# Performance work log

Hardware: AMD Instinct MI355X
Metric: run time of the kernel (lower is better)

Reference implementation:

```python
import jax, jax.numpy as jnp
import numpy as np

GROUPS = 8
EPS = 1e-5


def setup_inputs() -> dict:
    key = jax.random.key(0)
    ks = jax.random.split(key, 7)
    b, c, h, w = 32, 256, 32, 32
    x = jax.random.normal(ks[0], (b, c, h, w), dtype=jnp.float32)
    gn_weight = jax.random.normal(ks[1], (c,), dtype=jnp.float32) * 0.02 + 1.0
    gn_bias = jax.random.normal(ks[2], (c,), dtype=jnp.float32) * 0.02
    w_qkv = jax.random.normal(ks[3], (3 * c, c), dtype=jnp.float32) / np.sqrt(c)
    b_qkv = jax.random.normal(ks[4], (3 * c,), dtype=jnp.float32) * 0.01
    w_out = jax.random.normal(ks[5], (c, c), dtype=jnp.float32) / np.sqrt(c)
    b_out = jax.random.normal(ks[6], (c,), dtype=jnp.float32) * 0.01
    return {"x": x, "gn_weight": gn_weight, "gn_bias": gn_bias,
            "w_qkv": w_qkv, "b_qkv": b_qkv, "w_out": w_out, "b_out": b_out}


def group_norm(x, weight, bias):
    b, c, h, w = x.shape
    xg = x.reshape(b, GROUPS, c // GROUPS, h, w)
    mean = jnp.mean(xg, axis=(2, 3, 4), keepdims=True)
    var = jnp.var(xg, axis=(2, 3, 4), keepdims=True)
    xg = (xg - mean) * jax.lax.rsqrt(var + EPS)
    x = xg.reshape(b, c, h, w)
    return x * weight[None, :, None, None] + bias[None, :, None, None]


def reference(x, gn_weight, gn_bias, w_qkv, b_qkv, w_out, b_out):
    b, c, h, w = x.shape
    x_norm = group_norm(x, gn_weight, gn_bias)
    # 1x1 conv == channel matmul: (b, 3c, h, w)
    qkv = jnp.einsum('oc,bchw->bohw', w_qkv, x_norm) + b_qkv[None, :, None, None]
    q, k, v = jnp.split(qkv, 3, axis=1)
    hw = h * w
    q = q.reshape(b, c, hw)  # used transposed: (b, hw, c)
    k = k.reshape(b, c, hw)
    v = v.reshape(b, c, hw)
    scale = 1.0 / jnp.sqrt(jnp.float32(c))
    attn = jax.nn.softmax(jnp.einsum('bcs,bct->bst', q, k) * scale, axis=-1)  # (b, hw, hw)
    out = jnp.einsum('bst,bct->bcs', attn, v).reshape(b, c, h, w)
    out = jnp.einsum('oc,bchw->bohw', w_out, out) + b_out[None, :, None, None]
    return out + x
```

## Files before the change

### kernel.cpp

```cpp
#include <hip/hip_runtime.h>
#include <hip/hip_bf16.h>


typedef __bf16 bf16x8 __attribute__((ext_vector_type(8)));
typedef __bf16 bf16x4 __attribute__((ext_vector_type(4)));
typedef __bf16 bf16x2 __attribute__((ext_vector_type(2)));
typedef float f32x4 __attribute__((ext_vector_type(4)));
typedef float f32x16 __attribute__((ext_vector_type(16)));

#define MFMA16(a, b, c) __builtin_amdgcn_mfma_f32_16x16x32_bf16(a, b, c, 0, 0, 0)
#define MFMA32(a, b, c) __builtin_amdgcn_mfma_f32_32x32x16_bf16(a, b, c, 0, 0, 0)

#define GLD16(gsrc_, ldst_)                                                                  \
    __builtin_amdgcn_global_load_lds((const __attribute__((address_space(1))) void*)(gsrc_), \
                                     (__attribute__((address_space(3))) void*)(ldst_), 16, 0, 0)

__global__ __launch_bounds__(512) void gn_kernel(const float* __restrict__ x,
                                                 const float* __restrict__ gw,
                                                 const float* __restrict__ gb,
                                                 __bf16* __restrict__ xnT,
                                                 const float* __restrict__ wqkv,
                                                 const float* __restrict__ wout,
                                                 __bf16* __restrict__ wbf) {
    __shared__ float red[16];
    __shared__ float stats[2];
    __shared__ __bf16 Lds[512][40];
    const int b = blockIdx.x >> 3, g = blockIdx.x & 7;
    const size_t base = ((size_t)b * 256 + g * 32) * 1024;
    const float* xp = x + base;
    const int t = threadIdx.x;

    {
        int widx = (blockIdx.x * 512 + t) * 2;
        const float* wsrc = (widx < 196608) ? (wqkv + widx) : (wout + (widx - 196608));
        float2 wv = *(const float2*)wsrc;
        bf16x2 wo;
        wo[0] = (__bf16)wv.x; wo[1] = (__bf16)wv.y;
        *(bf16x2*)&wbf[widx] = wo;
    }

    float s = 0.f, s2 = 0.f;
    #pragma unroll
    for (int i = 0; i < 8; i++) {
        int j = i * 512 + t;
        float4 v0 = *(const float4*)(xp + (size_t)j * 8);
        float4 v1 = *(const float4*)(xp + (size_t)j * 8 + 4);
        s  += v0.x + v0.y + v0.z + v0.w + v1.x + v1.y + v1.z + v1.w;
        s2 += v0.x*v0.x + v0.y*v0.y + v0.z*v0.z + v0.w*v0.w
            + v1.x*v1.x + v1.y*v1.y + v1.z*v1.z + v1.w*v1.w;
    }
    #pragma unroll
    for (int o = 32; o > 0; o >>= 1) { s += __shfl_down(s, o, 64); s2 += __shfl_down(s2, o, 64); }
    const int wv = t >> 6;
    if ((t & 63) == 0) { red[wv * 2] = s; red[wv * 2 + 1] = s2; }
    __syncthreads();
    if (t == 0) {
        float ts = 0.f, ts2 = 0.f;
        for (int w = 0; w < 8; w++) { ts += red[w * 2]; ts2 += red[w * 2 + 1]; }
        float mean = ts / 32768.f;
        float var = ts2 / 32768.f - mean * mean;
        stats[0] = mean; stats[1] = rsqrtf(var + 1e-5f);
    }
    __syncthreads();
    const float mean = stats[0], inv = stats[1];

    const int c = t >> 4;
    const int so = (t & 15) * 2;
    const float ga = gw[g * 32 + c], be = gb[g * 32 + c];

    for (int chunk = 0; chunk < 1024; chunk += 512) {
        #pragma unroll
        for (int i = 0; i < 16; i++) {
            int sl = so + i * 32;
            float2 v = *(const float2*)(xp + (size_t)c * 1024 + chunk + sl);
            Lds[sl][c]     = (__bf16)((v.x - mean) * inv * ga + be);
            Lds[sl + 1][c] = (__bf16)((v.y - mean) * inv * ga + be);
        }
        __syncthreads();
        {
            int sl = t;
            #pragma unroll
            for (int u = 0; u < 4; u++) {
                bf16x8 vv = *(const bf16x8*)&Lds[sl][u * 8];
                *(bf16x8*)&xnT[((size_t)b * 1024 + chunk + sl) * 256 + g * 32 + u * 8] = vv;
            }
        }
        __syncthreads();
    }
}

#define GEMM64G_BODY(ArowBase_, BrowBase_)                                              \
    f32x4 acc[4][4] = {};                                                               \
    for (int kk = 0; kk < 256; kk += 64) {                                              \
        _Pragma("unroll")                                                               \
        for (int i = 0; i < 4; i++) {                                                   \
            const int ch = wave * 4 + i;                                                \
            const int r = ch * 8 + (lane >> 3);                                         \
            const int sw = ((lane & 7) ^ (r & 7)) * 8;                                  \
            GLD16((ArowBase_) + (size_t)r * 256 + kk + sw, (char*)&As[0][0] + ch * 1024); \
            GLD16((BrowBase_) + (size_t)r * 256 + kk + sw, (char*)&Bs[0][0] + ch * 1024); \
        }                                                                               \
        __syncthreads();                                                                \
        _Pragma("unroll")                                                               \
        for (int kh = 0; kh < 2; kh++) {                                                \
            bf16x8 af[4], bfv[4];                                                       \
            _Pragma("unroll")                                                           \
            for (int im = 0; im < 4; im++) {                                            \
                const int row = wm + im * 16 + l16;                                     \
                af[im] = *(const bf16x8*)&As[row][(((kh * 4 + quad) ^ (row & 7)) * 8)]; \
            }                                                                           \
            _Pragma("unroll")                                                           \
            for (int in = 0; in < 4; in++) {                                            \
                const int row = wn + in * 16 + l16;                                     \
                bfv[in] = *(const bf16x8*)&Bs[row][(((kh * 4 + quad) ^ (row & 7)) * 8)]; \
            }                                                                           \
            _Pragma("unroll")                                                           \
            for (int im = 0; im < 4; im++)                                              \
                _Pragma("unroll")                                                       \
                for (int in = 0; in < 4; in++)                                          \
                    acc[im][in] = MFMA16(af[im], bfv[in], acc[im][in]);                 \
        }                                                                               \
        __syncthreads();                                                                \
    }

__global__ __launch_bounds__(256) void qkv_gemm(const __bf16* __restrict__ wbf,
                                                const float* __restrict__ bias,
                                                const __bf16* __restrict__ xnT,
                                                __bf16* __restrict__ qtr,
                                                __bf16* __restrict__ ktr,
                                                __bf16* __restrict__ vbuf) {
    __shared__ union {
        struct { __bf16 A[128][64]; __bf16 B[128][64]; } g;
        __bf16 ct[128][136];
    } sm;
    const int b = blockIdx.z;
    const int n0 = blockIdx.x * 128, m0 = blockIdx.y * 128;
    const int t = threadIdx.x;
    const int wave = t >> 6, lane = t & 63, quad = lane >> 4, l16 = lane & 15;
    const int wm = (wave & 1) * 64, wn = (wave >> 1) * 64;
    const __bf16* arow = wbf + (size_t)m0 * 256;
    const __bf16* brow = xnT + ((size_t)b * 1024 + n0) * 256;
    auto As = sm.g.A;
    auto Bs = sm.g.B;

    GEMM64G_BODY(arow, brow)

    if (m0 < 512) {
        #pragma unroll
        for (int im = 0; im < 4; im++) {
            #pragma unroll
            for (int in = 0; in < 4; in++) {
                int ob = m0 + wm + im * 16 + quad * 4;
                bf16x4 ov;
                #pragma unroll
                for (int r = 0; r < 4; r++) ov[r] = (__bf16)(acc[im][in][r] + bias[ob + r]);
                *(bf16x4*)&sm.ct[wn + in * 16 + l16][wm + im * 16 + quad * 4] = ov;
            }
        }
        __syncthreads();
        {
            const int rbase = t >> 2, cf = t & 3;
            #pragma unroll
            for (int rr = 0; rr < 2; rr++) {
                int row = rbase + rr * 64;
                int sg = n0 + row;
                __bf16* dst = (m0 < 256) ? &qtr[((size_t)b * 1024 + sg) * 256 + m0]
                                         : &ktr[((size_t)b * 1024 + sg) * 256 + (m0 - 256)];
                #pragma unroll
                for (int u = 0; u < 4; u++) {
                    int colb = cf * 8 + u * 32;
                    *(bf16x8*)&dst[colb] = *(const bf16x8*)&sm.ct[row][colb];
                }
            }
        }
    } else {
        #pragma unroll
        for (int im = 0; im < 4; im++) {
            #pragma unroll
            for (int in = 0; in < 4; in++) {
                int cl = wm + im * 16 + quad * 4;
                int tl = wn + in * 16 + l16;
                #pragma unroll
                for (int r = 0; r < 4; r++)
                    sm.ct[cl + r][tl] = (__bf16)(acc[im][in][r] + bias[m0 + cl + r]);
            }
        }
        __syncthreads();
        {
            const int row = t >> 1, tc = (t & 1) * 64;
            const int cglob = m0 - 512 + row;
            __bf16* dst = &vbuf[((size_t)b * 256 + cglob) * 1024 + n0 + tc];
            #pragma unroll
            for (int u = 0; u < 8; u++)
                *(bf16x8*)&dst[u * 8] = *(const bf16x8*)&sm.ct[row][tc + u * 8];
        }
    }
}

__global__ __launch_bounds__(512, 2) void attn_kernel(const __bf16* __restrict__ qtr,
                                                      const __bf16* __restrict__ ktr,
                                                      const __bf16* __restrict__ vbuf,
                                                      __bf16* __restrict__ aoT) {
    __shared__ __bf16 Kt[2][32][260];
    __shared__ __bf16 Vs[2][256][36];
    __shared__ bf16x8 Pl[4][2][2][64];
    __shared__ float Lred[4][2][32];
    const int b = blockIdx.x;
    const int tid = threadIdx.x;
    const int wave = tid >> 6, lane = tid & 63, half = lane >> 5, l31 = lane & 31;
    const int pair = wave & 3, th = wave >> 2;
    const int s0 = blockIdx.y * 128 + pair * 32;
    const float kscale = 0.09016844f;

    bf16x8 aq[16];
    #pragma unroll
    for (int ks = 0; ks < 16; ks++)
        aq[ks] = *(const bf16x8*)&qtr[((size_t)b * 1024 + s0 + l31) * 256 + ks * 16 + half * 8];

    const int k_row = tid >> 3;
    const int k_cb  = (tid & 7) * 8;
    const int v_c   = tid >> 1;
    const int v_th  = tid & 1;
    const size_t kbase = (size_t)b * 1024 * 256;
    const size_t vbase = (size_t)b * 256 * 1024;

    float l_acc = 0.f;
    f32x16 o_acc[4] = {};

    bf16x8 kpre[4], vpre[4];
    #pragma unroll
    for (int u = 0; u < 4; u++) {
        kpre[u] = *(const bf16x8*)&ktr[kbase + (size_t)k_row * 256 + k_cb + u * 64];
        vpre[u] = *(const bf16x8*)&vbuf[vbase + (size_t)v_c * 1024 + v_th * 32 + u * 8];
    }

    for (int it = 0; it < 16; it++) {
        #pragma unroll
        for (int u = 0; u < 4; u++)
            *(bf16x8*)&Kt[k_row >> 5][k_row & 31][k_cb + u * 64] = kpre[u];
        #pragma unroll
        for (int u = 0; u < 4; u++) {
            const bf16x4* hv = (const bf16x4*)&vpre[u];
            const int sbase = (u >> 1) * 16 + (u & 1) * 4;
            *(bf16x4*)&Vs[v_th][v_c][sbase]     = hv[0];
            *(bf16x4*)&Vs[v_th][v_c][sbase + 8] = hv[1];
        }
        __syncthreads();
        if (it < 15) {
            const int t1 = (it + 1) * 64;
            #pragma unroll
            for (int u = 0; u < 4; u++) {
                kpre[u] = *(const bf16x8*)&ktr[kbase + (size_t)(t1 + k_row) * 256 + k_cb + u * 64];
                vpre[u] = *(const bf16x8*)&vbuf[vbase + (size_t)v_c * 1024 + t1 + v_th * 32 + u * 8];
            }
        }

        f32x16 sc_a = {}, sc_b = {};
        __builtin_amdgcn_s_setprio(1);
        #pragma unroll
        for (int ks = 0; ks < 8; ks++) {
            bf16x8 bk0 = *(const bf16x8*)&Kt[th][l31][ks * 16 + half * 8];
            bf16x8 bk1 = *(const bf16x8*)&Kt[th][l31][(ks + 8) * 16 + half * 8];
            sc_a = MFMA32(bk0, aq[ks], sc_a);
            sc_b = MFMA32(bk1, aq[ks + 8], sc_b);
        }
        __builtin_amdgcn_s_setprio(0);

        bf16x8 pf0, pf1;
        #pragma unroll
        for (int r = 0; r < 8; r++) {
            float p = exp2f((sc_a[r] + sc_b[r]) * kscale);
            l_acc += p;
            pf0[r] = (__bf16)p;
        }
        #pragma unroll
        for (int r = 8; r < 16; r++) {
            float p = exp2f((sc_a[r] + sc_b[r]) * kscale);
            l_acc += p;
            pf1[r - 8] = (__bf16)p;
        }
        Pl[pair][th][0][lane] = pf0;
        Pl[pair][th][1][lane] = pf1;
        __syncthreads();
        bf16x8 pp0 = Pl[pair][1 - th][0][lane];
        bf16x8 pp1 = Pl[pair][1 - th][1][lane];

        bf16x8 ap[4];
        if (th == 0) { ap[0] = pf0; ap[1] = pf1; ap[2] = pp0; ap[3] = pp1; }
        else         { ap[0] = pp0; ap[1] = pp1; ap[2] = pf0; ap[3] = pf1; }

        __builtin_amdgcn_s_setprio(1);
        #pragma unroll
        for (int n = 0; n < 4; n++) {
            int c = th * 128 + n * 32 + l31;
            #pragma unroll
            for (int kc = 0; kc < 4; kc++) {
                bf16x8 bv = *(const bf16x8*)&Vs[kc >> 1][c][(kc & 1) * 16 + half * 8];
                o_acc[n] = MFMA32(ap[kc], bv, o_acc[n]);
            }
        }
        __builtin_amdgcn_s_setprio(0);
        __syncthreads();
    }

    l_acc += __shfl_xor(l_acc, 32, 64);
    if (lane < 32) Lred[pair][th][l31] = l_acc;
    __syncthreads();
    #pragma unroll
    for (int r = 0; r < 16; r++) {
        int row = (r & 3) + 8 * (r >> 2) + 4 * half;
        float rinv = 1.0f / (Lred[pair][0][row] + Lred[pair][1][row]);
        #pragma unroll
        for (int n = 0; n < 4; n++) {
            int c = th * 128 + n * 32 + l31;
            aoT[((size_t)b * 1024 + s0 + row) * 256 + c] = (__bf16)(o_acc[n][r] * rinv);
        }
    }
}

__global__ __launch_bounds__(256) void proj_gemm(const __bf16* __restrict__ wbf_out,
                                                 const float* __restrict__ bias,
                                                 const __bf16* __restrict__ aoT,
                                                 const float* __restrict__ resid,
                                                 float* __restrict__ Out) {
    __shared__ union {
        struct { __bf16 A[128][64]; __bf16 B[128][64]; } g;
        float cf[64][132];
    } sm;
    const int b = blockIdx.z;
    const int n0 = blockIdx.x * 128, m0 = blockIdx.y * 128;
    const int t = threadIdx.x;
    const int wave = t >> 6, lane = t & 63, quad = lane >> 4, l16 = lane & 15;
    const int wm = (wave & 1) * 64, wn = (wave >> 1) * 64;
    const __bf16* arow = wbf_out + (size_t)m0 * 256;
    const __bf16* brow = aoT + ((size_t)b * 1024 + n0) * 256;
    auto As = sm.g.A;
    auto Bs = sm.g.B;

    GEMM64G_BODY(arow, brow)

    for (int h = 0; h < 2; h++) {
        if ((wave & 1) == h) {
            #pragma unroll
            for (int im = 0; im < 4; im++)
                #pragma unroll
                for (int in = 0; in < 4; in++)
                    #pragma unroll
                    for (int r = 0; r < 4; r++)
                        sm.cf[im * 16 + quad * 4 + r][wn + in * 16 + l16] = acc[im][in][r];
        }
        __syncthreads();
        {
            const int rloc = t >> 2, cq = (t & 3) * 4;
            const int o = m0 + h * 64 + rloc;
            const float bo = bias[o];
            const float* rrow = &resid[((size_t)b * 256 + o) * 1024 + n0];
            float* orow = &Out[((size_t)b * 256 + o) * 1024 + n0];
            #pragma unroll
            for (int u = 0; u < 8; u++) {
                int col = cq + u * 16;
                f32x4 cv = *(const f32x4*)&sm.cf[rloc][col];
                float4 rv = *(const float4*)&rrow[col];
                float4 ov;
                ov.x = cv[0] + bo + rv.x;
                ov.y = cv[1] + bo + rv.y;
                ov.z = cv[2] + bo + rv.z;
                ov.w = cv[3] + bo + rv.w;
                *(float4*)&orow[col] = ov;
            }
        }
        __syncthreads();
    }
}

extern "C" void kernel_launch(void* const* d_in, const int* in_sizes, int n_in,
                              void* d_out, int out_size, void* d_ws, size_t ws_size,
                              hipStream_t stream) {
    const float* x    = (const float*)d_in[0];
    const float* gw   = (const float*)d_in[1];
    const float* gb   = (const float*)d_in[2];
    const float* wqkv = (const float*)d_in[3];
    const float* bqkv = (const float*)d_in[4];
    const float* wout = (const float*)d_in[5];
    const float* bout = (const float*)d_in[6];
    float* out = (float*)d_out;

    const size_t T16 = (size_t)32 * 1024 * 256;
    __bf16* xnT  = (__bf16*)d_ws;
    __bf16* qtr  = xnT + T16;
    __bf16* ktr  = qtr + T16;
    __bf16* vbuf = ktr + T16;
    __bf16* aoT  = vbuf + T16;
    __bf16* wbf  = aoT + T16;

    gn_kernel<<<dim3(256), 512, 0, stream>>>(x, gw, gb, xnT, wqkv, wout, wbf);
    qkv_gemm<<<dim3(8, 6, 32), 256, 0, stream>>>(wbf, bqkv, xnT, qtr, ktr, vbuf);
    attn_kernel<<<dim3(32, 8), 512, 0, stream>>>(qtr, ktr, vbuf, aoT);
    proj_gemm<<<dim3(8, 2, 32), 256, 0, stream>>>(wbf + 196608, bout, aoT, x, out);
}
```

Before: 190.7 us.

## Split group norm into stats and apply kernels; remap GEMM blocks per XCD

The single 256-block group-norm kernel becomes two kernels: a 2048-block partial-stats pass (which also converts the weights to bf16) and a 2048-block apply/transpose pass that reduces the partial sums itself. This raises parallelism across the GPU's CUs, at the cost of one extra launch and reading x twice. The QKV and projection GEMMs also remap their block IDs so that consecutive tiles sharing operand panels land on the same XCD, which should improve L2 reuse.

New measurement: 186.4 us. -2.3%, faster.

```diff
diff --git a/kernel.cpp b/kernel.cpp
--- a/kernel.cpp
+++ b/kernel.cpp
@@ -4,7 +4,6 @@
 
 typedef __bf16 bf16x8 __attribute__((ext_vector_type(8)));
 typedef __bf16 bf16x4 __attribute__((ext_vector_type(4)));
-typedef __bf16 bf16x2 __attribute__((ext_vector_type(2)));
 typedef float f32x4 __attribute__((ext_vector_type(4)));
 typedef float f32x16 __attribute__((ext_vector_type(16)));
 
@@ -15,78 +14,72 @@
     __builtin_amdgcn_global_load_lds((const __attribute__((address_space(1))) void*)(gsrc_), \
                                      (__attribute__((address_space(3))) void*)(ldst_), 16, 0, 0)
 
-__global__ __launch_bounds__(512) void gn_kernel(const float* __restrict__ x,
-                                                 const float* __restrict__ gw,
-                                                 const float* __restrict__ gb,
-                                                 __bf16* __restrict__ xnT,
-                                                 const float* __restrict__ wqkv,
-                                                 const float* __restrict__ wout,
-                                                 __bf16* __restrict__ wbf) {
-    __shared__ float red[16];
-    __shared__ float stats[2];
-    __shared__ __bf16 Lds[512][40];
-    const int b = blockIdx.x >> 3, g = blockIdx.x & 7;
-    const size_t base = ((size_t)b * 256 + g * 32) * 1024;
-    const float* xp = x + base;
-    const int t = threadIdx.x;
-
-    {
-        int widx = (blockIdx.x * 512 + t) * 2;
-        const float* wsrc = (widx < 196608) ? (wqkv + widx) : (wout + (widx - 196608));
-        float2 wv = *(const float2*)wsrc;
-        bf16x2 wo;
-        wo[0] = (__bf16)wv.x; wo[1] = (__bf16)wv.y;
-        *(bf16x2*)&wbf[widx] = wo;
-    }
-
+__global__ __launch_bounds__(256) void gn_stats(const float* __restrict__ x,
+                                                float* __restrict__ stats,
+                                                const float* __restrict__ wqkv,
+                                                const float* __restrict__ wout,
+                                                __bf16* __restrict__ wbf) {
+    const int bid = blockIdx.x, t = threadIdx.x;
+    if (bid < 128) {
+        int idx = (bid * 256 + t) * 8;
+        const float* src = (idx < 196608) ? (wqkv + idx) : (wout + (idx - 196608));
+        float4 v0 = *(const float4*)src;
+        float4 v1 = *(const float4*)(src + 4);
+        bf16x8 o;
+        o[0] = (__bf16)v0.x; o[1] = (__bf16)v0.y; o[2] = (__bf16)v0.z; o[3] = (__bf16)v0.w;
+        o[4] = (__bf16)v1.x; o[5] = (__bf16)v1.y; o[6] = (__bf16)v1.z; o[7] = (__bf16)v1.w;
+        *(bf16x8*)&wbf[idx] = o;
+    }
+    const int bg = bid >> 3, part = bid & 7;
+    const float* xp = x + (size_t)bg * 32768 + part * 4096;
     float s = 0.f, s2 = 0.f;
     #pragma unroll
-    for (int i = 0; i < 8; i++) {
-        int j = i * 512 + t;
-        float4 v0 = *(const float4*)(xp + (size_t)j * 8);
-        float4 v1 = *(const float4*)(xp + (size_t)j * 8 + 4);
-        s  += v0.x + v0.y + v0.z + v0.w + v1.x + v1.y + v1.z + v1.w;
-        s2 += v0.x*v0.x + v0.y*v0.y + v0.z*v0.z + v0.w*v0.w
-            + v1.x*v1.x + v1.y*v1.y + v1.z*v1.z + v1.w*v1.w;
+    for (int i = 0; i < 4; i++) {
+        float4 v = *(const float4*)(xp + (i * 256 + t) * 4);
+        s  += v.x + v.y + v.z + v.w;
+        s2 += v.x*v.x + v.y*v.y + v.z*v.z + v.w*v.w;
     }
     #pragma unroll
     for (int o = 32; o > 0; o >>= 1) { s += __shfl_down(s, o, 64); s2 += __shfl_down(s2, o, 64); }
+    __shared__ float red[8];
     const int wv = t >> 6;
     if ((t & 63) == 0) { red[wv * 2] = s; red[wv * 2 + 1] = s2; }
     __syncthreads();
     if (t == 0) {
-        float ts = 0.f, ts2 = 0.f;
-        for (int w = 0; w < 8; w++) { ts += red[w * 2]; ts2 += red[w * 2 + 1]; }
-        float mean = ts / 32768.f;
-        float var = ts2 / 32768.f - mean * mean;
-        stats[0] = mean; stats[1] = rsqrtf(var + 1e-5f);
-    }
+        float ts  = red[0] + red[2] + red[4] + red[6];
+        float ts2 = red[1] + red[3] + red[5] + red[7];
+        stats[bg * 16 + part * 2]     = ts;
+        stats[bg * 16 + part * 2 + 1] = ts2;
+    }
+}
+
+__global__ __launch_bounds__(512) void gn_apply(const float* __restrict__ x,
+                                                const float* __restrict__ stats,
+                                                const float* __restrict__ gw,
+                                                const float* __restrict__ gb,
+                                                __bf16* __restrict__ xnT) {
+    const int bid = blockIdx.x;
+    const int bg = bid >> 3, part = bid & 7;
+    const int b = bg >> 3, g = bg & 7;
+    const int t = threadIdx.x;
+    float ts = 0.f, ts2 = 0.f;
+    #pragma unroll
+    for (int p = 0; p < 8; p++) { ts += stats[bg * 16 + p * 2]; ts2 += stats[bg * 16 + p * 2 + 1]; }
+    const float mean = ts / 32768.f;
+    const float inv = rsqrtf(ts2 / 32768.f - mean * mean + 1e-5f);
+    __shared__ __bf16 Lds[128][48];
+    const int c = t >> 4, ss = (t & 15) * 8;
+    const float ga = gw[g * 32 + c], be = gb[g * 32 + c];
+    const float* xp = x + (((size_t)b * 256 + g * 32 + c) * 1024) + part * 128 + ss;
+    float4 v0 = *(const float4*)xp;
+    float4 v1 = *(const float4*)(xp + 4);
+    float vv[8] = {v0.x, v0.y, v0.z, v0.w, v1.x, v1.y, v1.z, v1.w};
+    #pragma unroll
+    for (int i = 0; i < 8; i++) Lds[ss + i][c] = (__bf16)((vv[i] - mean) * inv * ga + be);
     __syncthreads();
-    const float mean = stats[0], inv = stats[1];
-
-    const int c = t >> 4;
-    const int so = (t & 15) * 2;
-    const float ga = gw[g * 32 + c], be = gb[g * 32 + c];
-
-    for (int chunk = 0; chunk < 1024; chunk += 512) {
-        #pragma unroll
-        for (int i = 0; i < 16; i++) {
-            int sl = so + i * 32;
-            float2 v = *(const float2*)(xp + (size_t)c * 1024 + chunk + sl);
-            Lds[sl][c]     = (__bf16)((v.x - mean) * inv * ga + be);
-            Lds[sl + 1][c] = (__bf16)((v.y - mean) * inv * ga + be);
-        }
-        __syncthreads();
-        {
-            int sl = t;
-            #pragma unroll
-            for (int u = 0; u < 4; u++) {
-                bf16x8 vv = *(const bf16x8*)&Lds[sl][u * 8];
-                *(bf16x8*)&xnT[((size_t)b * 1024 + chunk + sl) * 256 + g * 32 + u * 8] = vv;
-            }
-        }
-        __syncthreads();
-    }
+    const int row = t >> 2, cb = (t & 3) * 8;
+    bf16x8 ov = *(const bf16x8*)&Lds[row][cb];
+    *(bf16x8*)&xnT[((size_t)b * 1024 + part * 128 + row) * 256 + g * 32 + cb] = ov;
 }
 
 #define GEMM64G_BODY(ArowBase_, BrowBase_)                                              \
@@ -133,8 +126,12 @@
         struct { __bf16 A[128][64]; __bf16 B[128][64]; } g;
         __bf16 ct[128][136];
     } sm;
-    const int b = blockIdx.z;
-    const int n0 = blockIdx.x * 128, m0 = blockIdx.y * 128;
+    const int lin = blockIdx.x + ((blockIdx.y + blockIdx.z * 6) << 3);
+    const int xcd = lin & 7, idx = lin >> 3;
+    const int gwk = xcd * 192 + idx;
+    const int mt = gwk % 6, panel = gwk / 6;
+    const int b = panel >> 3;
+    const int n0 = (panel & 7) * 128, m0 = mt * 128;
     const int t = threadIdx.x;
     const int wave = t >> 6, lane = t & 63, quad = lane >> 4, l16 = lane & 15;
     const int wm = (wave & 1) * 64, wn = (wave >> 1) * 64;
@@ -327,8 +324,12 @@
         struct { __bf16 A[128][64]; __bf16 B[128][64]; } g;
         float cf[64][132];
     } sm;
-    const int b = blockIdx.z;
-    const int n0 = blockIdx.x * 128, m0 = blockIdx.y * 128;
+    const int lin = blockIdx.x + ((blockIdx.y + blockIdx.z * 2) << 3);
+    const int xcd = lin & 7, idx = lin >> 3;
+    const int gwk = xcd * 64 + idx;
+    const int mt = gwk & 1, panel = gwk >> 1;
+    const int b = panel >> 3;
+    const int n0 = (panel & 7) * 128, m0 = mt * 128;
     const int t = threadIdx.x;
     const int wave = t >> 6, lane = t & 63, quad = lane >> 4, l16 = lane & 15;
     const int wm = (wave & 1) * 64, wn = (wave >> 1) * 64;
@@ -392,8 +393,10 @@
     __bf16* vbuf = ktr + T16;
     __bf16* aoT  = vbuf + T16;
     __bf16* wbf  = aoT + T16;
-
-    gn_kernel<<<dim3(256), 512, 0, stream>>>(x, gw, gb, xnT, wqkv, wout, wbf);
+    float* gstats = (float*)(wbf + 262144);
+
+    gn_stats<<<dim3(2048), 256, 0, stream>>>(x, gstats, wqkv, wout, wbf);
+    gn_apply<<<dim3(2048), 512, 0, stream>>>(x, gstats, gw, gb, xnT);
     qkv_gemm<<<dim3(8, 6, 32), 256, 0, stream>>>(wbf, bqkv, xnT, qtr, ktr, vbuf);
     attn_kernel<<<dim3(32, 8), 512, 0, stream>>>(qtr, ktr, vbuf, aoT);
     proj_gemm<<<dim3(8, 2, 32), 256, 0, stream>>>(wbf + 196608, bout, aoT, x, out);
```
